# Optimization experiments

Measured on AMD Instinct MI355X. Metric: run time of the kernel, lower is better.

## Reference

```python
import jax, jax.numpy as jnp
import numpy as np

B, T, E, H = 2, 4096, 1024, 16
D = E // H
EPS = 1e-6


def setup_inputs() -> dict:
    key = jax.random.key(0)
    ks = jax.random.split(key, 9)
    s = 1.0 / np.sqrt(E)
    return {
        "x": jax.random.normal(ks[0], (B, T, E), dtype=jnp.float32),
        "wq": jax.random.uniform(ks[1], (E, E), jnp.float32, -s, s),
        "bq": jax.random.uniform(ks[2], (E,), jnp.float32, -s, s),
        "wk": jax.random.uniform(ks[3], (E, E), jnp.float32, -s, s),
        "bk": jax.random.uniform(ks[4], (E,), jnp.float32, -s, s),
        "wv": jax.random.uniform(ks[5], (E, E), jnp.float32, -s, s),
        "bv": jax.random.uniform(ks[6], (E,), jnp.float32, -s, s),
        "wo": jax.random.uniform(ks[7], (E, E), jnp.float32, -s, s),
        "bo": jax.random.uniform(ks[8], (E,), jnp.float32, -s, s),
    }


def _feature_map(x):
    # elu(x) + 1
    return jnp.where(x > 0, x + 1.0, jnp.exp(x))


def reference(x, wq, bq, wk, bk, wv, bv, wo, bo):
    b, t, e = x.shape
    q = _feature_map(x @ wq + bq).reshape(b, t, H, D)
    k = _feature_map(x @ wk + bk).reshape(b, t, H, D)
    v = (x @ wv + bv).reshape(b, t, H, D)

    # time-major for the recurrence: [T, B, H, D]
    qT = jnp.moveaxis(q, 1, 0)
    kT = jnp.moveaxis(k, 1, 0)
    vT = jnp.moveaxis(v, 1, 0)

    S0 = jnp.zeros((b, H, D, D), dtype=x.dtype)  # running sum of k \otimes v
    z0 = jnp.zeros((b, H, D), dtype=x.dtype)     # running sum of k

    def step(carry, qkv):
        S, z = carry
        qt, kt, vt = qkv
        S = S + jnp.einsum('bhd,bhe->bhde', kt, vt)
        z = z + kt
        num = jnp.einsum('bhd,bhde->bhe', qt, S)
        den = jnp.einsum('bhd,bhd->bh', qt, z)[..., None] + EPS
        return (S, z), num / den

    _, outT = jax.lax.scan(step, (S0, z0), (qT, kT, vT))  # [T, B, H, D]
    out = jnp.moveaxis(outT, 0, 1).reshape(b, t, e)
    return out @ wo + bo
```

## Files before the change

### kernel.cpp

```cpp
#include <hip/hip_runtime.h>
#include <hip/hip_bf16.h>
#include <cstdint>
#include <cstddef>

#define B_   2
#define T_   4096
#define E_   1024
#define H_   16
#define D_   64
#define M_   (B_ * T_)
#define KDIM 1024
#define NDIM 1024
#define EPSC 1e-6f
#define CT   128
#define NC   (T_ / CT)

typedef __attribute__((ext_vector_type(8))) short bf16x8;
typedef __attribute__((ext_vector_type(4))) float f32x4;

__device__ __forceinline__ float bf2f(uint32_t u) {
    union { uint32_t u; float f; } x; x.u = u << 16; return x.f;
}
__device__ __forceinline__ unsigned short f2bf(float f) {
    union { float f; uint32_t u; } x; x.f = f;
    uint32_t r = x.u + 0x7fffu + ((x.u >> 16) & 1u);
    return (unsigned short)(r >> 16);
}
__device__ __forceinline__ void gload16(const void* g, void* l) {
    __builtin_amdgcn_global_load_lds(
        (const __attribute__((address_space(1))) void*)g,
        (__attribute__((address_space(3))) void*)l, 16, 0, 0);
}

__global__ __launch_bounds__(256) void conv_bf16(
    const float* __restrict__ in, unsigned short* __restrict__ out)
{
    const int i = blockIdx.x * 256 + threadIdx.x;
    const float4* p = (const float4*)in;
    float4 a = p[i * 2], b = p[i * 2 + 1];
    ushort4 o0 = make_ushort4(f2bf(a.x), f2bf(a.y), f2bf(a.z), f2bf(a.w));
    ushort4 o1 = make_ushort4(f2bf(b.x), f2bf(b.y), f2bf(b.z), f2bf(b.w));
    *(ushort4*)&out[(size_t)i * 8] = o0;
    *(ushort4*)&out[(size_t)i * 8 + 4] = o1;
}

__global__ __launch_bounds__(256) void transpose_w4(
    const float* __restrict__ w0, const float* __restrict__ w1,
    const float* __restrict__ w2, const float* __restrict__ w3,
    unsigned short* __restrict__ o0, unsigned short* __restrict__ o1,
    unsigned short* __restrict__ o2, unsigned short* __restrict__ o3)
{
    const float* src; unsigned short* dst;
    switch (blockIdx.z) {
        case 0: src = w0; dst = o0; break;
        case 1: src = w1; dst = o1; break;
        case 2: src = w2; dst = o2; break;
        default: src = w3; dst = o3; break;
    }
    __shared__ float tile[64][65];
    const int t = threadIdx.x, tx = t & 63, ty = t >> 6;
    const int r0 = blockIdx.y * 64, c0 = blockIdx.x * 64;
#pragma unroll
    for (int i = 0; i < 16; ++i)
        tile[ty + i * 4][tx] = src[(size_t)(r0 + ty + i * 4) * KDIM + c0 + tx];
    __syncthreads();
#pragma unroll
    for (int i = 0; i < 16; ++i)
        dst[(size_t)(c0 + ty + i * 4) * KDIM + r0 + tx] = f2bf(tile[tx][ty + i * 4]);
}

__global__ __launch_bounds__(512, 2) void gemm_qkv_p(
    const unsigned short* __restrict__ A,
    const unsigned short* __restrict__ Wt,
    const float* __restrict__ bq, const float* __restrict__ bk,
    const float* __restrict__ bv,
    unsigned short* __restrict__ qb,  unsigned short* __restrict__ kb,
    unsigned short* __restrict__ ktb, unsigned short* __restrict__ vtb)
{
    __shared__ char lds[98304];

    const int tid  = threadIdx.x;
    const int lane = tid & 63;
    const int w    = tid >> 6;
    const int wm   = w >> 1;
    const int wn   = w & 1;
    const int lo   = lane & 15, hi = lane >> 4;

    const int orig = blockIdx.x;
    const int swz  = (orig & 7) * 96 + (orig >> 3);
    const int bx = swz % 24;
    const int by = swz / 24;
    const int row0 = by * 256;
    const int col0 = bx * 128;

    int sr, skE;
    { int X = tid * 16; int Y = X ^ (((X >> 7) & 7) << 4);
      sr = Y >> 7; skE = (Y & 127) >> 1; }
    const unsigned short* pa = A  + (size_t)(row0 + sr) * KDIM + skE;
    const unsigned short* pb = Wt + (size_t)(col0 + sr) * KDIM + skE;

#define BUFA(p) (lds + (p) * 32768)
#define BUFB(p) (lds + 65536 + (p) * 16384)
#define STGA(t) { char* d_ = BUFA((t) & 1) + tid * 16;                        \
    _Pragma("unroll") for (int ch = 0; ch < 4; ++ch)                          \
        gload16(pa + (size_t)ch * 64 * KDIM + (t) * 64, d_ + ch * 8192); }
#define STGB(t) { char* d_ = BUFB((t) & 1) + tid * 16;                        \
    _Pragma("unroll") for (int ch = 0; ch < 2; ++ch)                          \
        gload16(pb + (size_t)ch * 64 * KDIM + (t) * 64, d_ + ch * 8192); }

    const int koff0 = (hi * 16)       ^ ((lane & 7) << 4);
    const int koff1 = (64 + hi * 16)  ^ ((lane & 7) << 4);

    f32x4 acc[4][4] = {};
    const int NT = KDIM / 64;

    STGA(0); STGB(0); STGA(1);
    asm volatile("s_waitcnt vmcnt(4)" ::: "memory");
    __builtin_amdgcn_s_barrier();

#pragma unroll 2
    for (int t = 0; t < NT; ++t) {
        const char* bA = BUFA(t & 1);
        const char* bB = BUFB(t & 1);

        if (t + 1 < NT) STGB(t + 1);

        bf16x8 af[4][2], bfr[4][2];
#pragma unroll
        for (int m = 0; m < 4; ++m) {
            const char* p = bA + (wm * 64 + m * 16 + lo) * 128;
            af[m][0] = *(const bf16x8*)(p + koff0);
            af[m][1] = *(const bf16x8*)(p + koff1);
        }
#pragma unroll
        for (int n = 0; n < 4; ++n) {
            const char* p = bB + (wn * 64 + n * 16 + lo) * 128;
            bfr[n][0] = *(const bf16x8*)(p + koff0);
            bfr[n][1] = *(const bf16x8*)(p + koff1);
        }
        __builtin_amdgcn_s_setprio(1);
#pragma unroll
        for (int kk = 0; kk < 2; ++kk)
#pragma unroll
            for (int m = 0; m < 4; ++m)
#pragma unroll
                for (int n = 0; n < 4; ++n)
                    acc[m][n] = __builtin_amdgcn_mfma_f32_16x16x32_bf16(
                        af[m][kk], bfr[n][kk], acc[m][n], 0, 0, 0);
        __builtin_amdgcn_s_setprio(0);

        asm volatile("s_waitcnt lgkmcnt(0)" ::: "memory");
        __builtin_amdgcn_s_barrier();

        if (t + 2 < NT) {
            STGA(t + 2);
            asm volatile("s_waitcnt vmcnt(4)" ::: "memory");
        } else {
            asm volatile("s_waitcnt vmcnt(0)" ::: "memory");
        }
        __builtin_amdgcn_s_barrier();
    }
#undef STGA
#undef STGB
#undef BUFA
#undef BUFB

    unsigned short* ep = (unsigned short*)lds;
    const int matid = bx >> 3;
    const float* bias = (matid == 0) ? bq : (matid == 1) ? bk : bv;
#pragma unroll
    for (int n = 0; n < 4; ++n) {
        const int lcol = wn * 64 + n * 16 + lo;
        const float bval = bias[(bx & 7) * 128 + lcol];
#pragma unroll
        for (int m = 0; m < 4; ++m) {
            const int lr0 = wm * 64 + m * 16 + hi * 4;
#pragma unroll
            for (int j = 0; j < 4; ++j) {
                float v = acc[m][n][j] + bval;
                if (matid <= 1) v = (v > 0.f) ? (v + 1.f) : __expf(v);
                ep[(lr0 + j) * 136 + lcol] = f2bf(v);
            }
        }
    }
    __syncthreads();

    const int b   = row0 >> 12;
    const int tg0 = row0 & (T_ - 1);
    const int h0  = (bx & 7) * 2;

    if (matid <= 1) {
        unsigned short* dst0 = (matid == 0) ? qb : kb;
#pragma unroll
        for (int it = 0; it < 8; ++it) {
            const int vid = it * 512 + tid;
            const int head = vid >> 11;
            const int rem = vid & 2047;
            const int tr = rem >> 3, c8 = rem & 7;
            uint4 v = *(const uint4*)&ep[tr * 136 + head * 64 + c8 * 8];
            *(uint4*)&dst0[((size_t)((b * H_ + h0 + head) * T_) + tg0 + tr) * D_
                           + c8 * 8] = v;
        }
    }
    if (matid >= 1) {
        unsigned short* dstT = (matid == 1) ? ktb : vtb;
#pragma unroll
        for (int it = 0; it < 8; ++it) {
            const int vid = it * 512 + tid;
            const int head = vid >> 11;
            const int rem = vid & 2047;
            const int d = rem & 63, t8 = rem >> 6;
            unsigned short vals[8];
#pragma unroll
            for (int i = 0; i < 8; ++i)
                vals[i] = ep[(t8 * 8 + i) * 136 + head * 64 + d];
            *(uint4*)&dstT[((size_t)((b * H_ + h0 + head) * D_) + d) * T_
                           + tg0 + t8 * 8] = *(const uint4*)vals;
        }
    }
}

__global__ __launch_bounds__(256) void gemm_out(
    const unsigned short* __restrict__ A,
    const unsigned short* __restrict__ Bt,
    const float* __restrict__ bias, float* __restrict__ outf)
{
    __shared__ unsigned short As[128 * 32];
    __shared__ unsigned short Bs[128 * 32];

    const int tid  = threadIdx.x;
    const int lane = tid & 63;
    const int wave = tid >> 6;
    const int wr = wave >> 1, wc = wave & 1;
    const int orig = blockIdx.x;
    const int swz  = (orig & 7) * 64 + (orig >> 3);
    const int bx = swz & 7, by = swz >> 3;
    const int row0 = by * 128;
    const int col0 = bx * 128;

    f32x4 acc[4][4] = {};

    const unsigned short* Ag = A  + (size_t)(row0 + (tid >> 2)) * KDIM + (tid & 3) * 8;
    const unsigned short* Bg = Bt + (size_t)(col0 + (tid >> 2)) * KDIM + (tid & 3) * 8;
    unsigned short* AsW = As + wave * 512;
    unsigned short* BsW = Bs + wave * 512;

    const int fr = lane & 15;
    const int fk = (lane >> 4) * 8;

    for (int k0 = 0; k0 < KDIM; k0 += 32) {
        gload16(Ag + k0,              AsW);
        gload16(Ag + 64 * KDIM + k0,  AsW + 2048);
        gload16(Bg + k0,              BsW);
        gload16(Bg + 64 * KDIM + k0,  BsW + 2048);
        __syncthreads();

        bf16x8 af[4], bfr[4];
#pragma unroll
        for (int m = 0; m < 4; ++m)
            af[m] = *(const bf16x8*)&As[(wr * 64 + m * 16 + fr) * 32 + fk];
#pragma unroll
        for (int n = 0; n < 4; ++n)
            bfr[n] = *(const bf16x8*)&Bs[(wc * 64 + n * 16 + fr) * 32 + fk];
#pragma unroll
        for (int m = 0; m < 4; ++m)
#pragma unroll
            for (int n = 0; n < 4; ++n)
                acc[m][n] = __builtin_amdgcn_mfma_f32_16x16x32_bf16(
                    af[m], bfr[n], acc[m][n], 0, 0, 0);
        __syncthreads();
    }

    const int fcol = lane & 15;
    const int frow = (lane >> 4) * 4;
#pragma unroll
    for (int m = 0; m < 4; ++m) {
#pragma unroll
        for (int n = 0; n < 4; ++n) {
            const int col = col0 + wc * 64 + n * 16 + fcol;
            const float bval = bias[col];
            const int rbase = row0 + wr * 64 + m * 16 + frow;
#pragma unroll
            for (int j = 0; j < 4; ++j)
                outf[(size_t)(rbase + j) * NDIM + col] = acc[m][n][j] + bval;
        }
    }
}

__global__ __launch_bounds__(256) void chunk_sums_mfma(
    const unsigned short* __restrict__ Kt,
    const unsigned short* __restrict__ Vt,
    unsigned short* __restrict__ Sl,
    unsigned short* __restrict__ Zl)
{
    const int tid = threadIdx.x, lane = tid & 63, w = tid >> 6;
    const int lo = lane & 15, hi = lane >> 4;
    const int cid = blockIdx.x, bh = cid >> 5, c = cid & 31, t0 = c * CT;
    const unsigned short* kT = Kt + (size_t)bh * 64 * T_ + t0;
    const unsigned short* vT = Vt + (size_t)bh * 64 * T_ + t0;

    const bf16x8 ones8 = {0x3F80, 0x3F80, 0x3F80, 0x3F80,
                          0x3F80, 0x3F80, 0x3F80, 0x3F80};
    f32x4 acc[5] = {};
#pragma unroll
    for (int kt = 0; kt < 4; ++kt) {
        bf16x8 af = *(const bf16x8*)&kT[(size_t)(w * 16 + lo) * T_ + kt * 32 + hi * 8];
        bf16x8 bfr[5];
#pragma unroll
        for (int et = 0; et < 4; ++et)
            bfr[et] = *(const bf16x8*)&vT[(size_t)(et * 16 + lo) * T_ + kt * 32 + hi * 8];
        bfr[4] = ones8;
#pragma unroll
        for (int et = 0; et < 5; ++et)
            acc[et] = __builtin_amdgcn_mfma_f32_16x16x32_bf16(af, bfr[et], acc[et], 0, 0, 0);
    }
    unsigned short* sO = Sl + (size_t)cid * 4096;
    const int d0 = w * 16 + hi * 4;
#pragma unroll
    for (int et = 0; et < 4; ++et) {
        const int e = et * 16 + lo;
        ushort4 pk = make_ushort4(f2bf(acc[et][0]), f2bf(acc[et][1]),
                                  f2bf(acc[et][2]), f2bf(acc[et][3]));
        *(ushort4*)&sO[e * 64 + d0] = pk;
    }
    if (lo == 0) {
        ushort4 pk = make_ushort4(f2bf(acc[4][0]), f2bf(acc[4][1]),
                                  f2bf(acc[4][2]), f2bf(acc[4][3]));
        *(ushort4*)&Zl[(size_t)cid * 64 + d0] = pk;
    }
}

__global__ __launch_bounds__(256) void chunk_scan_bf(
    unsigned short* __restrict__ S, unsigned short* __restrict__ Z)
{
    const int bh = blockIdx.y;
    const int f0 = blockIdx.x * 512 + threadIdx.x * 2;
    float a0 = 0.f, a1 = 0.f;
    unsigned short* base = S + (size_t)bh * NC * 4096 + f0;
    for (int c = 0; c < NC; ++c) {
        uint32_t* p = (uint32_t*)(base + (size_t)c * 4096);
        uint32_t v = *p;
        float c0 = bf2f(v & 0xffffu), c1 = bf2f(v >> 16);
        *p = (uint32_t)f2bf(a0) | ((uint32_t)f2bf(a1) << 16);
        a0 += c0; a1 += c1;
    }
    if (blockIdx.x == 0 && threadIdx.x < 32) {
        float b0 = 0.f, b1 = 0.f;
        unsigned short* zb = Z + (size_t)bh * NC * 64 + threadIdx.x * 2;
        for (int c = 0; c < NC; ++c) {
            uint32_t* p = (uint32_t*)(zb + (size_t)c * 64);
            uint32_t v = *p;
            float c0 = bf2f(v & 0xffffu), c1 = bf2f(v >> 16);
            *p = (uint32_t)f2bf(b0) | ((uint32_t)f2bf(b1) << 16);
            b0 += c0; b1 += c1;
        }
    }
}

__global__ __launch_bounds__(256) void chunk_attn_mfma(
    const unsigned short* __restrict__ Qb,
    const unsigned short* __restrict__ Kb,
    const unsigned short* __restrict__ Vt,
    const unsigned short* __restrict__ SpT,
    const unsigned short* __restrict__ Zp,
    unsigned short* __restrict__ att)
{
    __shared__ unsigned short lds[128 * 128];

    const int tid = threadIdx.x;
    const int lane = tid & 63;
    const int w = tid >> 6;
    const int lo = lane & 15, hi = lane >> 4;
    const int cid = blockIdx.x;
    const int bh = cid >> 5, c = cid & 31;
    const int t0 = c * CT;

    const unsigned short* qB = Qb + ((size_t)bh * T_ + t0) * 64;
    const unsigned short* kB = Kb + ((size_t)bh * T_ + t0) * 64;
    const unsigned short* vB = Vt + (size_t)bh * 64 * T_ + t0;
    const unsigned short* sB = SpT + (size_t)cid * 4096;
    const unsigned short* zB = Zp + (size_t)cid * 64;

    bf16x8 ka[2][2];
#pragma unroll
    for (int si = 0; si < 2; ++si)
#pragma unroll
        for (int kt = 0; kt < 2; ++kt)
            ka[si][kt] = *(const bf16x8*)&kB[(w * 32 + si * 16 + lo) * 64 + kt * 32 + hi * 8];

    f32x4 pacc[2][8] = {};
#pragma unroll
    for (int ti = 0; ti < 8; ++ti) {
        if (ti >= 2 * w) {
#pragma unroll
            for (int kt = 0; kt < 2; ++kt) {
                bf16x8 qf = *(const bf16x8*)&qB[(ti * 16 + lo) * 64 + kt * 32 + hi * 8];
                pacc[0][ti] = __builtin_amdgcn_mfma_f32_16x16x32_bf16(
                    ka[0][kt], qf, pacc[0][ti], 0, 0, 0);
                if (ti >= 2 * w + 1)
                    pacc[1][ti] = __builtin_amdgcn_mfma_f32_16x16x32_bf16(
                        ka[1][kt], qf, pacc[1][ti], 0, 0, 0);
            }
        }
    }
#pragma unroll
    for (int ti = 0; ti < 8; ++ti) {
        if (ti >= 2 * w) {
            const int t = ti * 16 + lo;
#pragma unroll
            for (int si = 0; si < 2; ++si) {
                const int s0 = w * 32 + si * 16 + hi * 4;
                ushort4 pk;
                unsigned short* pe = (unsigned short*)&pk;
#pragma unroll
                for (int j = 0; j < 4; ++j)
                    pe[j] = (s0 + j <= t) ? f2bf(pacc[si][ti][j]) : (unsigned short)0;
                *(ushort4*)((char*)lds + t * 256 + ((s0 * 2) ^ ((t & 7) << 4))) = pk;
            }
        }
    }
    __syncthreads();

    const bf16x8 ones8 = {0x3F80, 0x3F80, 0x3F80, 0x3F80,
                          0x3F80, 0x3F80, 0x3F80, 0x3F80};
    f32x4 acc[2][5] = {};
#pragma unroll
    for (int kt = 0; kt < 6; ++kt) {
        const int skt = kt - 2;
        if (kt < 2 || skt <= w) {
            bf16x8 bfr[5];
            if (kt < 2) {
#pragma unroll
                for (int et = 0; et < 4; ++et)
                    bfr[et] = *(const bf16x8*)&sB[(et * 16 + lo) * 64 + kt * 32 + hi * 8];
                bfr[4] = *(const bf16x8*)&zB[kt * 32 + hi * 8];
            } else {
#pragma unroll
                for (int et = 0; et < 4; ++et)
                    bfr[et] = *(const bf16x8*)&vB[(size_t)(et * 16 + lo) * T_ + skt * 32 + hi * 8];
                bfr[4] = ones8;
            }
#pragma unroll
            for (int m = 0; m < 2; ++m) {
                const int t = w * 32 + m * 16 + lo;
                bf16x8 af;
                if (kt < 2)
                    af = *(const bf16x8*)&qB[t * 64 + kt * 32 + hi * 8];
                else
                    af = *(const bf16x8*)((char*)lds + t * 256 +
                         (((skt * 32 + hi * 8) * 2) ^ ((t & 7) << 4)));
#pragma unroll
                for (int et = 0; et < 5; ++et)
                    acc[m][et] = __builtin_amdgcn_mfma_f32_16x16x32_bf16(
                        af, bfr[et], acc[m][et], 0, 0, 0);
            }
        }
    }

    __syncthreads();
#pragma unroll
    for (int m = 0; m < 2; ++m) {
#pragma unroll
        for (int j = 0; j < 4; ++j) {
            const int t = w * 32 + m * 16 + hi * 4 + j;
            const float rden = 1.f / (acc[m][4][j] + EPSC);
#pragma unroll
            for (int et = 0; et < 4; ++et) {
                const int e = et * 16 + lo;
                *(unsigned short*)((char*)lds + t * 144 + e * 2) =
                    f2bf(acc[m][et][j] * rden);
            }
        }
    }
    __syncthreads();
    const int b = bh >> 4, h = bh & 15;
#pragma unroll
    for (int r = 0; r < 4; ++r) {
        const int vid = tid + r * 256;
        const int t = vid >> 3, eg = vid & 7;
        uint4 val = *(const uint4*)((const char*)lds + t * 144 + eg * 16);
        *(uint4*)&att[(size_t)(b * T_ + t0 + t) * E_ + h * 64 + eg * 8] = val;
    }
}

extern "C" void kernel_launch(void* const* d_in, const int* in_sizes, int n_in,
                              void* d_out, int out_size, void* d_ws, size_t ws_size,
                              hipStream_t stream)
{
    const float* x  = (const float*)d_in[0];
    const float* wq = (const float*)d_in[1];
    const float* bq = (const float*)d_in[2];
    const float* wk = (const float*)d_in[3];
    const float* bk = (const float*)d_in[4];
    const float* wv = (const float*)d_in[5];
    const float* bv = (const float*)d_in[6];
    const float* wo = (const float*)d_in[7];
    const float* bo = (const float*)d_in[8];
    float* out = (float*)d_out;

    char* ws = (char*)d_ws;
    unsigned short* qb  = (unsigned short*)(ws);
    unsigned short* kb  = (unsigned short*)(ws + (size_t)16 * 1024 * 1024);
    unsigned short* ktb = (unsigned short*)(ws + (size_t)32 * 1024 * 1024);
    unsigned short* vtb = (unsigned short*)(ws + (size_t)48 * 1024 * 1024);
    unsigned short* xb  = (unsigned short*)(ws + (size_t)64 * 1024 * 1024);
    unsigned short* attb = xb;
    unsigned short* Sl  = (unsigned short*)(ws + (size_t)80 * 1024 * 1024);
    unsigned short* Zl  = (unsigned short*)(ws + (size_t)88 * 1024 * 1024);
    unsigned short* wqT = (unsigned short*)(ws + (size_t)88 * 1024 * 1024 + 128 * 1024);
    unsigned short* wkT = wqT + (size_t)KDIM * NDIM;
    unsigned short* wvT = wkT + (size_t)KDIM * NDIM;
    unsigned short* woT = wvT + (size_t)KDIM * NDIM;

    conv_bf16<<<M_ * KDIM / (256 * 8), 256, 0, stream>>>(x, xb);
    transpose_w4<<<dim3(16, 16, 4), 256, 0, stream>>>(wq, wk, wv, wo,
                                                      wqT, wkT, wvT, woT);

    gemm_qkv_p<<<768, 512, 0, stream>>>(xb, wqT, bq, bk, bv, qb, kb, ktb, vtb);

    chunk_sums_mfma<<<B_ * H_ * NC, 256, 0, stream>>>(ktb, vtb, Sl, Zl);
    chunk_scan_bf<<<dim3(8, B_ * H_), 256, 0, stream>>>(Sl, Zl);
    chunk_attn_mfma<<<B_ * H_ * NC, 256, 0, stream>>>(qb, kb, vtb, Sl, Zl, attb);

    gemm_out<<<512, 256, 0, stream>>>(attb, woT, bo, out);
}
```

Measured before the change: 167.9 us.

## Rewrite QKV GEMM to 256 threads, single-buffered LDS with larger per-wave tiles

Replaces the 512-thread double-buffered QKV projection GEMM with a 256-thread version. Each wave now computes a 128x64 sub-tile, and K tiles are loaded into a single LDS buffer with plain __syncthreads between stages. This halves LDS use per block, allowing more blocks per CU, but drops the overlap of global loads with MFMA work. The epilogue is split into two passes that reuse the smaller LDS area. The larger accumulator array raises register pressure.

```diff
diff --git a/kernel.cpp b/kernel.cpp
--- a/kernel.cpp
+++ b/kernel.cpp
@@ -69,7 +69,7 @@
         dst[(size_t)(c0 + ty + i * 4) * KDIM + r0 + tx] = f2bf(tile[tx][ty + i * 4]);
 }
 
-__global__ __launch_bounds__(512, 2) void gemm_qkv_p(
+__global__ __launch_bounds__(256) void gemm_qkv_x(
     const unsigned short* __restrict__ A,
     const unsigned short* __restrict__ Wt,
     const float* __restrict__ bq, const float* __restrict__ bk,
@@ -77,7 +77,7 @@
     unsigned short* __restrict__ qb,  unsigned short* __restrict__ kb,
     unsigned short* __restrict__ ktb, unsigned short* __restrict__ vtb)
 {
-    __shared__ char lds[98304];
+    __shared__ char lds[49152];
 
     const int tid  = threadIdx.x;
     const int lane = tid & 63;
@@ -93,130 +93,115 @@
     const int row0 = by * 256;
     const int col0 = bx * 128;
 
-    int sr, skE;
-    { int X = tid * 16; int Y = X ^ (((X >> 7) & 7) << 4);
-      sr = Y >> 7; skE = (Y & 127) >> 1; }
-    const unsigned short* pa = A  + (size_t)(row0 + sr) * KDIM + skE;
-    const unsigned short* pb = Wt + (size_t)(col0 + sr) * KDIM + skE;
-
-#define BUFA(p) (lds + (p) * 32768)
-#define BUFB(p) (lds + 65536 + (p) * 16384)
-#define STGA(t) { char* d_ = BUFA((t) & 1) + tid * 16;                        \
-    _Pragma("unroll") for (int ch = 0; ch < 4; ++ch)                          \
-        gload16(pa + (size_t)ch * 64 * KDIM + (t) * 64, d_ + ch * 8192); }
-#define STGB(t) { char* d_ = BUFB((t) & 1) + tid * 16;                        \
-    _Pragma("unroll") for (int ch = 0; ch < 2; ++ch)                          \
-        gload16(pb + (size_t)ch * 64 * KDIM + (t) * 64, d_ + ch * 8192); }
-
-    const int koff0 = (hi * 16)       ^ ((lane & 7) << 4);
-    const int koff1 = (64 + hi * 16)  ^ ((lane & 7) << 4);
-
-    f32x4 acc[4][4] = {};
-    const int NT = KDIM / 64;
-
-    STGA(0); STGB(0); STGA(1);
-    asm volatile("s_waitcnt vmcnt(4)" ::: "memory");
-    __builtin_amdgcn_s_barrier();
-
-#pragma unroll 2
-    for (int t = 0; t < NT; ++t) {
-        const char* bA = BUFA(t & 1);
-        const char* bB = BUFB(t & 1);
-
-        if (t + 1 < NT) STGB(t + 1);
-
-        bf16x8 af[4][2], bfr[4][2];
-#pragma unroll
-        for (int m = 0; m < 4; ++m) {
-            const char* p = bA + (wm * 64 + m * 16 + lo) * 128;
-            af[m][0] = *(const bf16x8*)(p + koff0);
-            af[m][1] = *(const bf16x8*)(p + koff1);
-        }
-#pragma unroll
-        for (int n = 0; n < 4; ++n) {
-            const char* p = bB + (wn * 64 + n * 16 + lo) * 128;
-            bfr[n][0] = *(const bf16x8*)(p + koff0);
-            bfr[n][1] = *(const bf16x8*)(p + koff1);
-        }
-        __builtin_amdgcn_s_setprio(1);
-#pragma unroll
-        for (int kk = 0; kk < 2; ++kk)
-#pragma unroll
-            for (int m = 0; m < 4; ++m)
+    const unsigned short* pA[8];
+    const unsigned short* pB[4];
+#pragma unroll
+    for (int ch = 0; ch < 8; ++ch) {
+        int X = ch * 4096 + tid * 16;
+        int Y = X ^ (((X >> 7) & 7) << 4);
+        pA[ch] = A + (size_t)(row0 + (Y >> 7)) * KDIM + ((Y & 127) >> 1);
+    }
+#pragma unroll
+    for (int ch = 0; ch < 4; ++ch) {
+        int X = ch * 4096 + tid * 16;
+        int Y = X ^ (((X >> 7) & 7) << 4);
+        pB[ch] = Wt + (size_t)(col0 + (Y >> 7)) * KDIM + ((Y & 127) >> 1);
+    }
+
+    const int koff0 = (hi * 16)      ^ ((lo & 7) << 4);
+    const int koff1 = (64 + hi * 16) ^ ((lo & 7) << 4);
+
+    const char* ldsA = lds;
+    const char* ldsB = lds + 32768;
+
+    f32x4 acc[8][4] = {};
+
+    for (int t = 0; t < KDIM / 64; ++t) {
+#pragma unroll
+        for (int ch = 0; ch < 8; ++ch)
+            gload16(pA[ch] + t * 64, lds + ch * 4096 + tid * 16);
+#pragma unroll
+        for (int ch = 0; ch < 4; ++ch)
+            gload16(pB[ch] + t * 64, lds + 32768 + ch * 4096 + tid * 16);
+        __syncthreads();
+
+#pragma unroll
+        for (int kk = 0; kk < 2; ++kk) {
+            const int ko = kk ? koff1 : koff0;
+            bf16x8 af[8], bfr[4];
+#pragma unroll
+            for (int m = 0; m < 8; ++m)
+                af[m] = *(const bf16x8*)(ldsA + (wm * 128 + m * 16 + lo) * 128 + ko);
+#pragma unroll
+            for (int n = 0; n < 4; ++n)
+                bfr[n] = *(const bf16x8*)(ldsB + (wn * 64 + n * 16 + lo) * 128 + ko);
+#pragma unroll
+            for (int m = 0; m < 8; ++m)
 #pragma unroll
                 for (int n = 0; n < 4; ++n)
                     acc[m][n] = __builtin_amdgcn_mfma_f32_16x16x32_bf16(
-                        af[m][kk], bfr[n][kk], acc[m][n], 0, 0, 0);
-        __builtin_amdgcn_s_setprio(0);
-
-        asm volatile("s_waitcnt lgkmcnt(0)" ::: "memory");
-        __builtin_amdgcn_s_barrier();
-
-        if (t + 2 < NT) {
-            STGA(t + 2);
-            asm volatile("s_waitcnt vmcnt(4)" ::: "memory");
-        } else {
-            asm volatile("s_waitcnt vmcnt(0)" ::: "memory");
-        }
-        __builtin_amdgcn_s_barrier();
-    }
-#undef STGA
-#undef STGB
-#undef BUFA
-#undef BUFB
+                        af[m], bfr[n], acc[m][n], 0, 0, 0);
+        }
+        __syncthreads();
+    }
 
     unsigned short* ep = (unsigned short*)lds;
     const int matid = bx >> 3;
     const float* bias = (matid == 0) ? bq : (matid == 1) ? bk : bv;
-#pragma unroll
-    for (int n = 0; n < 4; ++n) {
-        const int lcol = wn * 64 + n * 16 + lo;
-        const float bval = bias[(bx & 7) * 128 + lcol];
-#pragma unroll
-        for (int m = 0; m < 4; ++m) {
-            const int lr0 = wm * 64 + m * 16 + hi * 4;
-#pragma unroll
-            for (int j = 0; j < 4; ++j) {
-                float v = acc[m][n][j] + bval;
-                if (matid <= 1) v = (v > 0.f) ? (v + 1.f) : __expf(v);
-                ep[(lr0 + j) * 136 + lcol] = f2bf(v);
-            }
-        }
-    }
-    __syncthreads();
-
     const int b   = row0 >> 12;
     const int tg0 = row0 & (T_ - 1);
     const int h0  = (bx & 7) * 2;
 
-    if (matid <= 1) {
-        unsigned short* dst0 = (matid == 0) ? qb : kb;
-#pragma unroll
-        for (int it = 0; it < 8; ++it) {
-            const int vid = it * 512 + tid;
-            const int head = vid >> 11;
-            const int rem = vid & 2047;
-            const int tr = rem >> 3, c8 = rem & 7;
-            uint4 v = *(const uint4*)&ep[tr * 136 + head * 64 + c8 * 8];
-            *(uint4*)&dst0[((size_t)((b * H_ + h0 + head) * T_) + tg0 + tr) * D_
-                           + c8 * 8] = v;
-        }
-    }
-    if (matid >= 1) {
-        unsigned short* dstT = (matid == 1) ? ktb : vtb;
-#pragma unroll
-        for (int it = 0; it < 8; ++it) {
-            const int vid = it * 512 + tid;
-            const int head = vid >> 11;
-            const int rem = vid & 2047;
-            const int d = rem & 63, t8 = rem >> 6;
-            unsigned short vals[8];
-#pragma unroll
-            for (int i = 0; i < 8; ++i)
-                vals[i] = ep[(t8 * 8 + i) * 136 + head * 64 + d];
-            *(uint4*)&dstT[((size_t)((b * H_ + h0 + head) * D_) + d) * T_
-                           + tg0 + t8 * 8] = *(const uint4*)vals;
-        }
+#pragma unroll
+    for (int pass = 0; pass < 2; ++pass) {
+        if (wm == pass) {
+#pragma unroll
+            for (int n = 0; n < 4; ++n) {
+                const int col = wn * 64 + n * 16 + lo;
+                const float bval = bias[(bx & 7) * 128 + col];
+#pragma unroll
+                for (int m = 0; m < 8; ++m) {
+#pragma unroll
+                    for (int j = 0; j < 4; ++j) {
+                        float v = acc[m][n][j] + bval;
+                        if (matid <= 1) v = (v > 0.f) ? (v + 1.f) : __expf(v);
+                        ep[(m * 16 + hi * 4 + j) * 136 + col] = f2bf(v);
+                    }
+                }
+            }
+        }
+        __syncthreads();
+
+        if (matid <= 1) {
+            unsigned short* dst0 = (matid == 0) ? qb : kb;
+#pragma unroll
+            for (int it = 0; it < 8; ++it) {
+                const int vid = it * 256 + tid;
+                const int head = vid >> 10;
+                const int rem = vid & 1023;
+                const int tr = rem >> 3, c8 = rem & 7;
+                uint4 v = *(const uint4*)&ep[tr * 136 + head * 64 + c8 * 8];
+                *(uint4*)&dst0[((size_t)((b * H_ + h0 + head) * T_)
+                                + tg0 + pass * 128 + tr) * D_ + c8 * 8] = v;
+            }
+        }
+        if (matid >= 1) {
+            unsigned short* dstT = (matid == 1) ? ktb : vtb;
+#pragma unroll
+            for (int it = 0; it < 8; ++it) {
+                const int vid = it * 256 + tid;
+                const int head = vid >> 10;
+                const int rem = vid & 1023;
+                const int d = rem & 63, t8 = rem >> 6;
+                unsigned short vals[8];
+#pragma unroll
+                for (int i = 0; i < 8; ++i)
+                    vals[i] = ep[(t8 * 8 + i) * 136 + head * 64 + d];
+                *(uint4*)&dstT[((size_t)((b * H_ + h0 + head) * D_) + d) * T_
+                               + tg0 + pass * 128 + t8 * 8] = *(const uint4*)vals;
+            }
+        }
+        __syncthreads();
     }
 }
 
@@ -516,7 +501,7 @@
     transpose_w4<<<dim3(16, 16, 4), 256, 0, stream>>>(wq, wk, wv, wo,
                                                       wqT, wkT, wvT, woT);
 
-    gemm_qkv_p<<<768, 512, 0, stream>>>(xb, wqT, bq, bk, bv, qb, kb, ktb, vtb);
+    gemm_qkv_x<<<768, 256, 0, stream>>>(xb, wqT, bq, bk, bv, qb, kb, ktb, vtb);
 
     chunk_sums_mfma<<<B_ * H_ * NC, 256, 0, stream>>>(ktb, vtb, Sl, Zl);
     chunk_scan_bf<<<dim3(8, B_ * H_), 256, 0, stream>>>(Sl, Zl);
```

Result: slower. 216.0 us (+28.7%).

## Replace output GEMM with pipelined double-buffered 256x128 tile kernel

Applied to the files above, without the earlier changes.

Rewrites the output projection GEMM to reuse the QKV GEMM's design: 512-thread blocks with 256x128 tiles, BK=64, XOR-swizzled LDS, double buffering that prefetches upcoming tiles while MFMAs run, and s_setprio around the MFMA block. This targets the old kernel's small 32-wide K steps and its two full barriers per step with no load/compute overlap. The grid drops to 256 blocks, which may leave CUs underused. The QKV GEMM block-index mapping also changes, grouping column tiles differently for cache locality.

```diff
diff --git a/kernel.cpp b/kernel.cpp
--- a/kernel.cpp
+++ b/kernel.cpp
@@ -87,9 +87,10 @@
     const int lo   = lane & 15, hi = lane >> 4;
 
     const int orig = blockIdx.x;
-    const int swz  = (orig & 7) * 96 + (orig >> 3);
-    const int bx = swz % 24;
-    const int by = swz / 24;
+    const int cs = orig & 7;
+    const int i6 = orig >> 3;
+    const int bx = cs * 3 + (i6 % 3);
+    const int by = i6 / 3;
     const int row0 = by * 256;
     const int col0 = bx * 128;
 
@@ -220,66 +221,105 @@
     }
 }
 
-__global__ __launch_bounds__(256) void gemm_out(
+__global__ __launch_bounds__(512, 2) void gemm_out_p(
     const unsigned short* __restrict__ A,
     const unsigned short* __restrict__ Bt,
     const float* __restrict__ bias, float* __restrict__ outf)
 {
-    __shared__ unsigned short As[128 * 32];
-    __shared__ unsigned short Bs[128 * 32];
+    __shared__ char lds[98304];
 
     const int tid  = threadIdx.x;
     const int lane = tid & 63;
-    const int wave = tid >> 6;
-    const int wr = wave >> 1, wc = wave & 1;
+    const int w    = tid >> 6;
+    const int wm   = w >> 1;
+    const int wn   = w & 1;
+    const int lo   = lane & 15, hi = lane >> 4;
+
     const int orig = blockIdx.x;
-    const int swz  = (orig & 7) * 64 + (orig >> 3);
-    const int bx = swz & 7, by = swz >> 3;
-    const int row0 = by * 128;
+    const int bx = orig & 7;
+    const int by = orig >> 3;
+    const int row0 = by * 256;
     const int col0 = bx * 128;
 
+    int sr, skE;
+    { int X = tid * 16; int Y = X ^ (((X >> 7) & 7) << 4);
+      sr = Y >> 7; skE = (Y & 127) >> 1; }
+    const unsigned short* pa = A  + (size_t)(row0 + sr) * KDIM + skE;
+    const unsigned short* pb = Bt + (size_t)(col0 + sr) * KDIM + skE;
+
+#define BUFA(p) (lds + (p) * 32768)
+#define BUFB(p) (lds + 65536 + (p) * 16384)
+#define STGA(t) { char* d_ = BUFA((t) & 1) + tid * 16;                        \
+    _Pragma("unroll") for (int ch = 0; ch < 4; ++ch)                          \
+        gload16(pa + (size_t)ch * 64 * KDIM + (t) * 64, d_ + ch * 8192); }
+#define STGB(t) { char* d_ = BUFB((t) & 1) + tid * 16;                        \
+    _Pragma("unroll") for (int ch = 0; ch < 2; ++ch)                          \
+        gload16(pb + (size_t)ch * 64 * KDIM + (t) * 64, d_ + ch * 8192); }
+
+    const int koff0 = (hi * 16)       ^ ((lane & 7) << 4);
+    const int koff1 = (64 + hi * 16)  ^ ((lane & 7) << 4);
+
     f32x4 acc[4][4] = {};
-
-    const unsigned short* Ag = A  + (size_t)(row0 + (tid >> 2)) * KDIM + (tid & 3) * 8;
-    const unsigned short* Bg = Bt + (size_t)(col0 + (tid >> 2)) * KDIM + (tid & 3) * 8;
-    unsigned short* AsW = As + wave * 512;
-    unsigned short* BsW = Bs + wave * 512;
-
-    const int fr = lane & 15;
-    const int fk = (lane >> 4) * 8;
-
-    for (int k0 = 0; k0 < KDIM; k0 += 32) {
-        gload16(Ag + k0,              AsW);
-        gload16(Ag + 64 * KDIM + k0,  AsW + 2048);
-        gload16(Bg + k0,              BsW);
-        gload16(Bg + 64 * KDIM + k0,  BsW + 2048);
-        __syncthreads();
-
-        bf16x8 af[4], bfr[4];
-#pragma unroll
-        for (int m = 0; m < 4; ++m)
-            af[m] = *(const bf16x8*)&As[(wr * 64 + m * 16 + fr) * 32 + fk];
-#pragma unroll
-        for (int n = 0; n < 4; ++n)
-            bfr[n] = *(const bf16x8*)&Bs[(wc * 64 + n * 16 + fr) * 32 + fk];
-#pragma unroll
-        for (int m = 0; m < 4; ++m)
-#pragma unroll
-            for (int n = 0; n < 4; ++n)
-                acc[m][n] = __builtin_amdgcn_mfma_f32_16x16x32_bf16(
-                    af[m], bfr[n], acc[m][n], 0, 0, 0);
-        __syncthreads();
-    }
-
-    const int fcol = lane & 15;
-    const int frow = (lane >> 4) * 4;
-#pragma unroll
-    for (int m = 0; m < 4; ++m) {
+    const int NT = KDIM / 64;
+
+    STGA(0); STGB(0); STGA(1);
+    asm volatile("s_waitcnt vmcnt(4)" ::: "memory");
+    __builtin_amdgcn_s_barrier();
+
+#pragma unroll 2
+    for (int t = 0; t < NT; ++t) {
+        const char* bA = BUFA(t & 1);
+        const char* bB = BUFB(t & 1);
+
+        if (t + 1 < NT) STGB(t + 1);
+
+        bf16x8 af[4][2], bfr[4][2];
+#pragma unroll
+        for (int m = 0; m < 4; ++m) {
+            const char* p = bA + (wm * 64 + m * 16 + lo) * 128;
+            af[m][0] = *(const bf16x8*)(p + koff0);
+            af[m][1] = *(const bf16x8*)(p + koff1);
+        }
 #pragma unroll
         for (int n = 0; n < 4; ++n) {
-            const int col = col0 + wc * 64 + n * 16 + fcol;
-            const float bval = bias[col];
-            const int rbase = row0 + wr * 64 + m * 16 + frow;
+            const char* p = bB + (wn * 64 + n * 16 + lo) * 128;
+            bfr[n][0] = *(const bf16x8*)(p + koff0);
+            bfr[n][1] = *(const bf16x8*)(p + koff1);
+        }
+        __builtin_amdgcn_s_setprio(1);
+#pragma unroll
+        for (int kk = 0; kk < 2; ++kk)
+#pragma unroll
+            for (int m = 0; m < 4; ++m)
+#pragma unroll
+                for (int n = 0; n < 4; ++n)
+                    acc[m][n] = __builtin_amdgcn_mfma_f32_16x16x32_bf16(
+                        af[m][kk], bfr[n][kk], acc[m][n], 0, 0, 0);
+        __builtin_amdgcn_s_setprio(0);
+
+        asm volatile("s_waitcnt lgkmcnt(0)" ::: "memory");
+        __builtin_amdgcn_s_barrier();
+
+        if (t + 2 < NT) {
+            STGA(t + 2);
+            asm volatile("s_waitcnt vmcnt(4)" ::: "memory");
+        } else {
+            asm volatile("s_waitcnt vmcnt(0)" ::: "memory");
+        }
+        __builtin_amdgcn_s_barrier();
+    }
+#undef STGA
+#undef STGB
+#undef BUFA
+#undef BUFB
+
+#pragma unroll
+    for (int n = 0; n < 4; ++n) {
+        const int col = col0 + wn * 64 + n * 16 + lo;
+        const float bval = bias[col];
+#pragma unroll
+        for (int m = 0; m < 4; ++m) {
+            const int rbase = row0 + wm * 64 + m * 16 + hi * 4;
 #pragma unroll
             for (int j = 0; j < 4; ++j)
                 outf[(size_t)(rbase + j) * NDIM + col] = acc[m][n][j] + bval;
@@ -522,5 +562,5 @@
     chunk_scan_bf<<<dim3(8, B_ * H_), 256, 0, stream>>>(Sl, Zl);
     chunk_attn_mfma<<<B_ * H_ * NC, 256, 0, stream>>>(qb, kb, vtb, Sl, Zl, attb);
 
-    gemm_out<<<512, 256, 0, stream>>>(attb, woT, bo, out);
-}
+    gemm_out_p<<<256, 512, 0, stream>>>(attb, woT, bo, out);
+}
```

Measured after the change: 170.7 us. Within noise of the previous version (+1.7%).

## Triple-buffer GEMM pipeline, reuse it for output projection, merge prep kernels

Applied to the files above, without the earlier changes.

The bf16 conversion of x and the weight transposes are merged into one prep launch. The QKV GEMM moves from double-buffered to triple-buffered LDS staging, with one barrier per k-step and 144KB of shared memory, which forces one block per CU. The output projection now uses the same templated 256x128 pipelined GEMM instead of the simpler 128x128 kernel, aiming to hide load latency better and cut launch count, at the cost of halving occupancy for the QKV GEMM.

```diff
diff --git a/kernel.cpp b/kernel.cpp
--- a/kernel.cpp
+++ b/kernel.cpp
@@ -32,24 +32,28 @@
         (__attribute__((address_space(3))) void*)l, 16, 0, 0);
 }
 
-__global__ __launch_bounds__(256) void conv_bf16(
-    const float* __restrict__ in, unsigned short* __restrict__ out)
-{
-    const int i = blockIdx.x * 256 + threadIdx.x;
-    const float4* p = (const float4*)in;
-    float4 a = p[i * 2], b = p[i * 2 + 1];
-    ushort4 o0 = make_ushort4(f2bf(a.x), f2bf(a.y), f2bf(a.z), f2bf(a.w));
-    ushort4 o1 = make_ushort4(f2bf(b.x), f2bf(b.y), f2bf(b.z), f2bf(b.w));
-    *(ushort4*)&out[(size_t)i * 8] = o0;
-    *(ushort4*)&out[(size_t)i * 8 + 4] = o1;
-}
-
-__global__ __launch_bounds__(256) void transpose_w4(
+__global__ __launch_bounds__(256) void prep(
+    const float* __restrict__ x, unsigned short* __restrict__ xb,
     const float* __restrict__ w0, const float* __restrict__ w1,
     const float* __restrict__ w2, const float* __restrict__ w3,
     unsigned short* __restrict__ o0, unsigned short* __restrict__ o1,
     unsigned short* __restrict__ o2, unsigned short* __restrict__ o3)
 {
+    const int t = threadIdx.x;
+    if (blockIdx.z == 4) {
+        const int bi = blockIdx.y * 16 + blockIdx.x;
+        const float4* p = (const float4*)x;
+#pragma unroll
+        for (int j = 0; j < 16; ++j) {
+            const int i = bi * 256 + t + j * 65536;
+            float4 a = p[i * 2], b = p[i * 2 + 1];
+            ushort4 q0 = make_ushort4(f2bf(a.x), f2bf(a.y), f2bf(a.z), f2bf(a.w));
+            ushort4 q1 = make_ushort4(f2bf(b.x), f2bf(b.y), f2bf(b.z), f2bf(b.w));
+            *(ushort4*)&xb[(size_t)i * 8] = q0;
+            *(ushort4*)&xb[(size_t)i * 8 + 4] = q1;
+        }
+        return;
+    }
     const float* src; unsigned short* dst;
     switch (blockIdx.z) {
         case 0: src = w0; dst = o0; break;
@@ -58,7 +62,7 @@
         default: src = w3; dst = o3; break;
     }
     __shared__ float tile[64][65];
-    const int t = threadIdx.x, tx = t & 63, ty = t >> 6;
+    const int tx = t & 63, ty = t >> 6;
     const int r0 = blockIdx.y * 64, c0 = blockIdx.x * 64;
 #pragma unroll
     for (int i = 0; i < 16; ++i)
@@ -69,15 +73,17 @@
         dst[(size_t)(c0 + ty + i * 4) * KDIM + r0 + tx] = f2bf(tile[tx][ty + i * 4]);
 }
 
-__global__ __launch_bounds__(512, 2) void gemm_qkv_p(
+template <int MODE>
+__global__ __launch_bounds__(512, 1) void gemm_tb(
     const unsigned short* __restrict__ A,
     const unsigned short* __restrict__ Wt,
     const float* __restrict__ bq, const float* __restrict__ bk,
     const float* __restrict__ bv,
     unsigned short* __restrict__ qb,  unsigned short* __restrict__ kb,
-    unsigned short* __restrict__ ktb, unsigned short* __restrict__ vtb)
-{
-    __shared__ char lds[98304];
+    unsigned short* __restrict__ ktb, unsigned short* __restrict__ vtb,
+    float* __restrict__ outf)
+{
+    __shared__ char lds[147456];
 
     const int tid  = threadIdx.x;
     const int lane = tid & 63;
@@ -86,10 +92,17 @@
     const int wn   = w & 1;
     const int lo   = lane & 15, hi = lane >> 4;
 
-    const int orig = blockIdx.x;
-    const int swz  = (orig & 7) * 96 + (orig >> 3);
-    const int bx = swz % 24;
-    const int by = swz / 24;
+    int bx, by;
+    if (MODE == 0) {
+        const int orig = blockIdx.x;
+        const int swz  = (orig & 7) * 96 + (orig >> 3);
+        bx = swz % 24;
+        by = swz / 24;
+    } else {
+        const int orig = blockIdx.x;
+        bx = orig & 7;
+        by = orig >> 3;
+    }
     const int row0 = by * 256;
     const int col0 = bx * 128;
 
@@ -99,14 +112,13 @@
     const unsigned short* pa = A  + (size_t)(row0 + sr) * KDIM + skE;
     const unsigned short* pb = Wt + (size_t)(col0 + sr) * KDIM + skE;
 
-#define BUFA(p) (lds + (p) * 32768)
-#define BUFB(p) (lds + 65536 + (p) * 16384)
-#define STGA(t) { char* d_ = BUFA((t) & 1) + tid * 16;                        \
-    _Pragma("unroll") for (int ch = 0; ch < 4; ++ch)                          \
-        gload16(pa + (size_t)ch * 64 * KDIM + (t) * 64, d_ + ch * 8192); }
-#define STGB(t) { char* d_ = BUFB((t) & 1) + tid * 16;                        \
-    _Pragma("unroll") for (int ch = 0; ch < 2; ++ch)                          \
-        gload16(pb + (size_t)ch * 64 * KDIM + (t) * 64, d_ + ch * 8192); }
+#define STG(t, da, db) {                                                      \
+    { char* d_ = (da) + tid * 16;                                             \
+      _Pragma("unroll") for (int ch = 0; ch < 4; ++ch)                        \
+        gload16(pa + (size_t)ch * 64 * KDIM + (t) * 64, d_ + ch * 8192); }    \
+    { char* d_ = (db) + tid * 16;                                             \
+      _Pragma("unroll") for (int ch = 0; ch < 2; ++ch)                        \
+        gload16(pb + (size_t)ch * 64 * KDIM + (t) * 64, d_ + ch * 8192); } }
 
     const int koff0 = (hi * 16)       ^ ((lane & 7) << 4);
     const int koff1 = (64 + hi * 16)  ^ ((lane & 7) << 4);
@@ -114,27 +126,28 @@
     f32x4 acc[4][4] = {};
     const int NT = KDIM / 64;
 
-    STGA(0); STGB(0); STGA(1);
-    asm volatile("s_waitcnt vmcnt(4)" ::: "memory");
+    char* pA0 = lds;           char* pB0 = lds + 98304;
+    char* pA1 = lds + 32768;   char* pB1 = lds + 114688;
+    char* pA2 = lds + 65536;   char* pB2 = lds + 131072;
+
+    STG(0, pA0, pB0);
+    STG(1, pA1, pB1);
+    asm volatile("s_waitcnt vmcnt(6)" ::: "memory");
     __builtin_amdgcn_s_barrier();
 
-#pragma unroll 2
     for (int t = 0; t < NT; ++t) {
-        const char* bA = BUFA(t & 1);
-        const char* bB = BUFB(t & 1);
-
-        if (t + 1 < NT) STGB(t + 1);
+        if (t + 2 < NT) STG(t + 2, pA2, pB2);
 
         bf16x8 af[4][2], bfr[4][2];
 #pragma unroll
         for (int m = 0; m < 4; ++m) {
-            const char* p = bA + (wm * 64 + m * 16 + lo) * 128;
+            const char* p = pA0 + (wm * 64 + m * 16 + lo) * 128;
             af[m][0] = *(const bf16x8*)(p + koff0);
             af[m][1] = *(const bf16x8*)(p + koff1);
         }
 #pragma unroll
         for (int n = 0; n < 4; ++n) {
-            const char* p = bB + (wn * 64 + n * 16 + lo) * 128;
+            const char* p = pB0 + (wn * 64 + n * 16 + lo) * 128;
             bfr[n][0] = *(const bf16x8*)(p + koff0);
             bfr[n][1] = *(const bf16x8*)(p + koff1);
         }
@@ -149,21 +162,31 @@
                         af[m][kk], bfr[n][kk], acc[m][n], 0, 0, 0);
         __builtin_amdgcn_s_setprio(0);
 
+        if (t + 2 < NT) { asm volatile("s_waitcnt vmcnt(6)" ::: "memory"); }
+        else            { asm volatile("s_waitcnt vmcnt(0)" ::: "memory"); }
         asm volatile("s_waitcnt lgkmcnt(0)" ::: "memory");
         __builtin_amdgcn_s_barrier();
 
-        if (t + 2 < NT) {
-            STGA(t + 2);
-            asm volatile("s_waitcnt vmcnt(4)" ::: "memory");
-        } else {
-            asm volatile("s_waitcnt vmcnt(0)" ::: "memory");
-        }
-        __builtin_amdgcn_s_barrier();
-    }
-#undef STGA
-#undef STGB
-#undef BUFA
-#undef BUFB
+        char* ta = pA0; pA0 = pA1; pA1 = pA2; pA2 = ta;
+        char* tb = pB0; pB0 = pB1; pB1 = pB2; pB2 = tb;
+    }
+#undef STG
+
+    if (MODE == 1) {
+#pragma unroll
+        for (int n = 0; n < 4; ++n) {
+            const int col = col0 + wn * 64 + n * 16 + lo;
+            const float bval = bq[col];
+#pragma unroll
+            for (int m = 0; m < 4; ++m) {
+                const int rbase = row0 + wm * 64 + m * 16 + hi * 4;
+#pragma unroll
+                for (int j = 0; j < 4; ++j)
+                    outf[(size_t)(rbase + j) * NDIM + col] = acc[m][n][j] + bval;
+            }
+        }
+        return;
+    }
 
     unsigned short* ep = (unsigned short*)lds;
     const int matid = bx >> 3;
@@ -216,73 +239,6 @@
                 vals[i] = ep[(t8 * 8 + i) * 136 + head * 64 + d];
             *(uint4*)&dstT[((size_t)((b * H_ + h0 + head) * D_) + d) * T_
                            + tg0 + t8 * 8] = *(const uint4*)vals;
-        }
-    }
-}
-
-__global__ __launch_bounds__(256) void gemm_out(
-    const unsigned short* __restrict__ A,
-    const unsigned short* __restrict__ Bt,
-    const float* __restrict__ bias, float* __restrict__ outf)
-{
-    __shared__ unsigned short As[128 * 32];
-    __shared__ unsigned short Bs[128 * 32];
-
-    const int tid  = threadIdx.x;
-    const int lane = tid & 63;
-    const int wave = tid >> 6;
-    const int wr = wave >> 1, wc = wave & 1;
-    const int orig = blockIdx.x;
-    const int swz  = (orig & 7) * 64 + (orig >> 3);
-    const int bx = swz & 7, by = swz >> 3;
-    const int row0 = by * 128;
-    const int col0 = bx * 128;
-
-    f32x4 acc[4][4] = {};
-
-    const unsigned short* Ag = A  + (size_t)(row0 + (tid >> 2)) * KDIM + (tid & 3) * 8;
-    const unsigned short* Bg = Bt + (size_t)(col0 + (tid >> 2)) * KDIM + (tid & 3) * 8;
-    unsigned short* AsW = As + wave * 512;
-    unsigned short* BsW = Bs + wave * 512;
-
-    const int fr = lane & 15;
-    const int fk = (lane >> 4) * 8;
-
-    for (int k0 = 0; k0 < KDIM; k0 += 32) {
-        gload16(Ag + k0,              AsW);
-        gload16(Ag + 64 * KDIM + k0,  AsW + 2048);
-        gload16(Bg + k0,              BsW);
-        gload16(Bg + 64 * KDIM + k0,  BsW + 2048);
-        __syncthreads();
-
-        bf16x8 af[4], bfr[4];
-#pragma unroll
-        for (int m = 0; m < 4; ++m)
-            af[m] = *(const bf16x8*)&As[(wr * 64 + m * 16 + fr) * 32 + fk];
-#pragma unroll
-        for (int n = 0; n < 4; ++n)
-            bfr[n] = *(const bf16x8*)&Bs[(wc * 64 + n * 16 + fr) * 32 + fk];
-#pragma unroll
-        for (int m = 0; m < 4; ++m)
-#pragma unroll
-            for (int n = 0; n < 4; ++n)
-                acc[m][n] = __builtin_amdgcn_mfma_f32_16x16x32_bf16(
-                    af[m], bfr[n], acc[m][n], 0, 0, 0);
-        __syncthreads();
-    }
-
-    const int fcol = lane & 15;
-    const int frow = (lane >> 4) * 4;
-#pragma unroll
-    for (int m = 0; m < 4; ++m) {
-#pragma unroll
-        for (int n = 0; n < 4; ++n) {
-            const int col = col0 + wc * 64 + n * 16 + fcol;
-            const float bval = bias[col];
-            const int rbase = row0 + wr * 64 + m * 16 + frow;
-#pragma unroll
-            for (int j = 0; j < 4; ++j)
-                outf[(size_t)(rbase + j) * NDIM + col] = acc[m][n][j] + bval;
         }
     }
 }
@@ -512,15 +468,16 @@
     unsigned short* wvT = wkT + (size_t)KDIM * NDIM;
     unsigned short* woT = wvT + (size_t)KDIM * NDIM;
 
-    conv_bf16<<<M_ * KDIM / (256 * 8), 256, 0, stream>>>(x, xb);
-    transpose_w4<<<dim3(16, 16, 4), 256, 0, stream>>>(wq, wk, wv, wo,
-                                                      wqT, wkT, wvT, woT);
-
-    gemm_qkv_p<<<768, 512, 0, stream>>>(xb, wqT, bq, bk, bv, qb, kb, ktb, vtb);
+    prep<<<dim3(16, 16, 5), 256, 0, stream>>>(x, xb, wq, wk, wv, wo,
+                                              wqT, wkT, wvT, woT);
+
+    gemm_tb<0><<<768, 512, 0, stream>>>(xb, wqT, bq, bk, bv,
+                                        qb, kb, ktb, vtb, nullptr);
 
     chunk_sums_mfma<<<B_ * H_ * NC, 256, 0, stream>>>(ktb, vtb, Sl, Zl);
     chunk_scan_bf<<<dim3(8, B_ * H_), 256, 0, stream>>>(Sl, Zl);
     chunk_attn_mfma<<<B_ * H_ * NC, 256, 0, stream>>>(qb, kb, vtb, Sl, Zl, attb);
 
-    gemm_out<<<512, 256, 0, stream>>>(attb, woT, bo, out);
-}
+    gemm_tb<1><<<256, 512, 0, stream>>>(attb, woT, bo, nullptr, nullptr,
+                                        nullptr, nullptr, nullptr, nullptr, out);
+}
```

Result: no change. 165.8 us (median of 3 runs) (-1.2%).
